# Optimization experiments

Hardware: AMD Instinct MI355X
Metric: run time of the kernel (lower is better)

## Reference

```python
import jax, jax.numpy as jnp
import numpy as np

N, F, H, E = 10000, 256, 256, 320000
TEMPERATURE = 1.0


def setup_inputs() -> dict:
    key = jax.random.key(0)
    k_x, k_ei, k_w1, k_b1, k_w2, k_b2 = jax.random.split(key, 6)
    x = jax.random.normal(k_x, (N, F), dtype=jnp.float32)
    edge_index = jax.random.randint(k_ei, (2, E), 0, N, dtype=jnp.int64)
    # PyTorch nn.Linear default init: U(-1/sqrt(fan_in), 1/sqrt(fan_in)), weight shape (out, in)
    lim1 = 1.0 / np.sqrt(2 * F)
    W1 = jax.random.uniform(k_w1, (H, 2 * F), dtype=jnp.float32, minval=-lim1, maxval=lim1)
    b1 = jax.random.uniform(k_b1, (H,), dtype=jnp.float32, minval=-lim1, maxval=lim1)
    lim2 = 1.0 / np.sqrt(H)
    W2 = jax.random.uniform(k_w2, (1, H), dtype=jnp.float32, minval=-lim2, maxval=lim2)
    b2 = jax.random.uniform(k_b2, (1,), dtype=jnp.float32, minval=-lim2, maxval=lim2)
    return {"x": x, "edge_index": edge_index, "W1": W1, "b1": b1, "W2": W2, "b2": b2}


def reference(x, edge_index, W1, b1, W2, b2):
    row, col = edge_index[0], edge_index[1]
    edge_feat = jnp.concatenate([x[row], x[col]], axis=-1)  # (E, 2F)
    h = jax.nn.relu(edge_feat @ W1.T + b1)                  # (E, H)
    logits = (h @ W2.T + b2).squeeze(-1)                    # (E,)
    m = jax.nn.sigmoid(logits / max(TEMPERATURE, 1e-6))
    return m
```

## Files before the change

kernel.cpp:

```cpp
#include <hip/hip_runtime.h>
#include <hip/hip_bf16.h>


typedef __attribute__((ext_vector_type(8))) short bf16x8;
typedef __attribute__((ext_vector_type(4))) float f32x4;

__device__ __forceinline__ unsigned short f2bf(float f) {
    __hip_bfloat16 h = __float2bfloat16(f);
    return *reinterpret_cast<unsigned short*>(&h);
}

__global__ __launch_bounds__(256) void convert_w(const float* __restrict__ w1,
                                                 unsigned short* __restrict__ wb,
                                                 int nw4) {
    int i = blockIdx.x * 256 + threadIdx.x;
    if (i < nw4) {
        float4 v = ((const float4*)w1)[i];
        ushort4 o = {f2bf(v.x), f2bf(v.y), f2bf(v.z), f2bf(v.w)};
        ((ushort4*)wb)[i] = o;
    }
}

__global__ __launch_bounds__(256) void gemm_mfma(const float* __restrict__ x,
                                                 const unsigned short* __restrict__ wb,
                                                 const float* __restrict__ b1,
                                                 unsigned short* __restrict__ uv,
                                                 int M) {
    __shared__ unsigned short As[2][16][40];

    const int t    = threadIdx.x;
    const int wave = t >> 6;
    const int lane = t & 63;
    const int lm   = lane & 15;
    const int lq   = lane >> 4;
    const int lk   = lq * 8;
    const int m0   = blockIdx.x * 16;

    const int srow = t >> 4;
    const int sk   = (t & 15) * 2;
    const int grow = m0 + srow;
    const float* sptr = x + (size_t)(grow < M ? grow : (M - 1)) * 256 + sk;

    const int half    = wave >> 1;
    const int colbase = wave * 128;
    const int rowbase = (wave & 1) * 128;
    const unsigned short* bpre =
        wb + (size_t)(rowbase + lm) * 512 + half * 256 + lk;

    f32x4 acc[8];
#pragma unroll
    for (int j = 0; j < 8; ++j) acc[j] = f32x4{0.f, 0.f, 0.f, 0.f};

    float2 apref = *(const float2*)(sptr);

#pragma unroll
    for (int it = 0; it < 8; ++it) {
        const int kt  = it * 32;
        const int cur = it & 1;

        unsigned int lo = ((unsigned int)f2bf(apref.x));
        unsigned int hi = ((unsigned int)f2bf(apref.y)) << 16;
        *(unsigned int*)&As[cur][srow][sk] = lo | hi;

        if (it < 7) apref = *(const float2*)(sptr + kt + 32);

        __syncthreads();

        bf16x8 a = *(const bf16x8*)&As[cur][lm][lk];

#pragma unroll
        for (int j = 0; j < 8; ++j) {
            bf16x8 b = *(const bf16x8*)(bpre + (size_t)j * 16 * 512 + kt);
            acc[j] = __builtin_amdgcn_mfma_f32_16x16x32_bf16(a, b, acc[j], 0, 0, 0);
        }
    }

    const int row0 = m0 + lq * 4;
#pragma unroll
    for (int j = 0; j < 8; ++j) {
        const int col  = colbase + j * 16 + lm;
        const float badd = half ? 0.f : b1[col];
#pragma unroll
        for (int r = 0; r < 4; ++r) {
            if (row0 + r < M)
                uv[(size_t)(row0 + r) * 512 + col] = f2bf(acc[j][r] + badd);
        }
    }
}

__global__ __launch_bounds__(256) void edge_kernel(const unsigned short* __restrict__ uv,
                                                   const int* __restrict__ ei,
                                                   const float* __restrict__ w2,
                                                   const float* __restrict__ b2p,
                                                   float* __restrict__ out, int E) {
    const int lane = threadIdx.x & 63;
    const int g = lane >> 4;
    const int c = lane & 15;
    const int wid = (blockIdx.x * blockDim.x + threadIdx.x) >> 6;
    const int nwav = (gridDim.x * blockDim.x) >> 6;
    const int nb = E >> 2;

    float w2r[16];
#pragma unroll
    for (int i = 0; i < 4; ++i)
        *(float4*)&w2r[i * 4] = *(const float4*)(w2 + c * 16 + i * 4);
    const float b2 = b2p[0];

    for (int b = wid; b < nb; b += nwav) {
        const int e = b * 4 + g;
        const int row = ei[e];
        const int col = ei[E + e];
        const unsigned int* up = (const unsigned int*)(uv + (size_t)row * 512 + c * 16);
        const unsigned int* vp = (const unsigned int*)(uv + (size_t)col * 512 + 256 + c * 16);

        unsigned int uw[8], vw[8];
        *(uint4*)&uw[0] = *(const uint4*)up;
        *(uint4*)&uw[4] = *(const uint4*)(up + 4);
        *(uint4*)&vw[0] = *(const uint4*)vp;
        *(uint4*)&vw[4] = *(const uint4*)(vp + 4);

        float2 p2 = {0.f, 0.f};
#pragma unroll
        for (int i = 0; i < 8; ++i) {
            float2 u2 = {__uint_as_float(uw[i] << 16),
                         __uint_as_float(uw[i] & 0xffff0000u)};
            float2 v2 = {__uint_as_float(vw[i] << 16),
                         __uint_as_float(vw[i] & 0xffff0000u)};
            float2 s2 = {u2.x + v2.x, u2.y + v2.y};
            s2.x = fmaxf(s2.x, 0.f);
            s2.y = fmaxf(s2.y, 0.f);
            p2.x = fmaf(s2.x, w2r[2 * i], p2.x);
            p2.y = fmaf(s2.y, w2r[2 * i + 1], p2.y);
        }
        float p = p2.x + p2.y;

#pragma unroll
        for (int off = 1; off < 16; off <<= 1)
            p += __shfl_xor(p, off, 64);

        if (c == 0) {
            out[e] = 1.f / (1.f + __expf(-(p + b2)));
        }
    }
}

extern "C" void kernel_launch(void* const* d_in, const int* in_sizes, int n_in,
                              void* d_out, int out_size, void* d_ws, size_t ws_size,
                              hipStream_t stream) {
    const float* x  = (const float*)d_in[0];
    const int*   ei = (const int*)d_in[1];
    const float* W1 = (const float*)d_in[2];
    const float* b1 = (const float*)d_in[3];
    const float* W2 = (const float*)d_in[4];
    const float* b2 = (const float*)d_in[5];
    float* out = (float*)d_out;

    const int N = in_sizes[0] / 256;
    const int E = in_sizes[1] / 2;

    unsigned short* uv = (unsigned short*)d_ws;
    unsigned short* wb = uv + (size_t)N * 512;

    const int nw4 = (256 * 512) / 4;
    convert_w<<<(nw4 + 255) / 256, 256, 0, stream>>>(W1, wb, nw4);

    gemm_mfma<<<(N + 15) / 16, 256, 0, stream>>>(x, wb, b1, uv, N);

    edge_kernel<<<2048, 256, 0, stream>>>(uv, ei, W2, b2, out, E);
}
```

Measured before the change: 131.0 us.

## Fuse weight convert, node GEMM and edge scoring into one cooperative kernel

Merges the three launches (weight bf16 conversion, per-node projection GEMM, per-edge scoring) into a single persistent cooperative kernel separated by grid-wide syncs. The GEMM becomes a grid-stride loop over row tiles. The edge loop now handles two edge batches per iteration so more gathers are in flight. This removes two launch gaps but adds grid.sync cost, and the persistent grid, which assumes 256 CUs, may be less occupied than the original per-kernel grids.

```diff
diff --git a/kernel.cpp b/kernel.cpp
--- a/kernel.cpp
+++ b/kernel.cpp
@@ -1,5 +1,8 @@
 #include <hip/hip_runtime.h>
 #include <hip/hip_bf16.h>
+#include <hip/hip_cooperative_groups.h>
+
+namespace cg = cooperative_groups;
 
 
 typedef __attribute__((ext_vector_type(8))) short bf16x8;
@@ -10,95 +13,87 @@
     return *reinterpret_cast<unsigned short*>(&h);
 }
 
-__global__ __launch_bounds__(256) void convert_w(const float* __restrict__ w1,
-                                                 unsigned short* __restrict__ wb,
-                                                 int nw4) {
-    int i = blockIdx.x * 256 + threadIdx.x;
-    if (i < nw4) {
-        float4 v = ((const float4*)w1)[i];
+__global__ __launch_bounds__(256, 4) void fused_kernel(
+        const float* __restrict__ x, const int* __restrict__ ei,
+        const float* __restrict__ W1, const float* __restrict__ b1,
+        const float* __restrict__ w2, const float* __restrict__ b2p,
+        float* __restrict__ out, unsigned short* __restrict__ uv,
+        unsigned short* __restrict__ wb, int M, int E) {
+    __shared__ __align__(16) unsigned short As[2][16][40];
+
+    cg::grid_group grid = cg::this_grid();
+    const int t   = threadIdx.x;
+    const int gid = blockIdx.x * 256 + t;
+
+    if (gid < 32768) {
+        float4 v = ((const float4*)W1)[gid];
         ushort4 o = {f2bf(v.x), f2bf(v.y), f2bf(v.z), f2bf(v.w)};
-        ((ushort4*)wb)[i] = o;
+        ((ushort4*)wb)[gid] = o;
     }
-}
-
-__global__ __launch_bounds__(256) void gemm_mfma(const float* __restrict__ x,
-                                                 const unsigned short* __restrict__ wb,
-                                                 const float* __restrict__ b1,
-                                                 unsigned short* __restrict__ uv,
-                                                 int M) {
-    __shared__ unsigned short As[2][16][40];
-
-    const int t    = threadIdx.x;
+    grid.sync();
+
     const int wave = t >> 6;
     const int lane = t & 63;
     const int lm   = lane & 15;
     const int lq   = lane >> 4;
     const int lk   = lq * 8;
-    const int m0   = blockIdx.x * 16;
-
     const int srow = t >> 4;
     const int sk   = (t & 15) * 2;
-    const int grow = m0 + srow;
-    const float* sptr = x + (size_t)(grow < M ? grow : (M - 1)) * 256 + sk;
-
     const int half    = wave >> 1;
     const int colbase = wave * 128;
     const int rowbase = (wave & 1) * 128;
     const unsigned short* bpre =
         wb + (size_t)(rowbase + lm) * 512 + half * 256 + lk;
 
-    f32x4 acc[8];
-#pragma unroll
-    for (int j = 0; j < 8; ++j) acc[j] = f32x4{0.f, 0.f, 0.f, 0.f};
-
-    float2 apref = *(const float2*)(sptr);
-
-#pragma unroll
-    for (int it = 0; it < 8; ++it) {
-        const int kt  = it * 32;
-        const int cur = it & 1;
-
-        unsigned int lo = ((unsigned int)f2bf(apref.x));
-        unsigned int hi = ((unsigned int)f2bf(apref.y)) << 16;
-        *(unsigned int*)&As[cur][srow][sk] = lo | hi;
-
-        if (it < 7) apref = *(const float2*)(sptr + kt + 32);
-
+    const int ntiles = (M + 15) / 16;
+    for (int mt = blockIdx.x; mt < ntiles; mt += gridDim.x) {
+        const int m0   = mt * 16;
+        const int grow = m0 + srow;
+        const float* sptr = x + (size_t)(grow < M ? grow : (M - 1)) * 256 + sk;
+
+        f32x4 acc[8];
+#pragma unroll
+        for (int j = 0; j < 8; ++j) acc[j] = f32x4{0.f, 0.f, 0.f, 0.f};
+
+        float2 apref = *(const float2*)(sptr);
+
+#pragma unroll
+        for (int it = 0; it < 8; ++it) {
+            const int kt  = it * 32;
+            const int cur = it & 1;
+            unsigned int lo = ((unsigned int)f2bf(apref.x));
+            unsigned int hi = ((unsigned int)f2bf(apref.y)) << 16;
+            *(unsigned int*)&As[cur][srow][sk] = lo | hi;
+            if (it < 7) apref = *(const float2*)(sptr + kt + 32);
+            __syncthreads();
+            bf16x8 a = *(const bf16x8*)&As[cur][lm][lk];
+#pragma unroll
+            for (int j = 0; j < 8; ++j) {
+                bf16x8 b = *(const bf16x8*)(bpre + (size_t)j * 16 * 512 + kt);
+                acc[j] = __builtin_amdgcn_mfma_f32_16x16x32_bf16(a, b, acc[j], 0, 0, 0);
+            }
+        }
+
+        const int row0 = m0 + lq * 4;
+#pragma unroll
+        for (int j = 0; j < 8; ++j) {
+            const int col  = colbase + j * 16 + lm;
+            const float badd = half ? 0.f : b1[col];
+#pragma unroll
+            for (int r = 0; r < 4; ++r) {
+                if (row0 + r < M)
+                    uv[(size_t)(row0 + r) * 512 + col] = f2bf(acc[j][r] + badd);
+            }
+        }
         __syncthreads();
-
-        bf16x8 a = *(const bf16x8*)&As[cur][lm][lk];
-
-#pragma unroll
-        for (int j = 0; j < 8; ++j) {
-            bf16x8 b = *(const bf16x8*)(bpre + (size_t)j * 16 * 512 + kt);
-            acc[j] = __builtin_amdgcn_mfma_f32_16x16x32_bf16(a, b, acc[j], 0, 0, 0);
-        }
     }
-
-    const int row0 = m0 + lq * 4;
-#pragma unroll
-    for (int j = 0; j < 8; ++j) {
-        const int col  = colbase + j * 16 + lm;
-        const float badd = half ? 0.f : b1[col];
-#pragma unroll
-        for (int r = 0; r < 4; ++r) {
-            if (row0 + r < M)
-                uv[(size_t)(row0 + r) * 512 + col] = f2bf(acc[j][r] + badd);
-        }
-    }
-}
-
-__global__ __launch_bounds__(256) void edge_kernel(const unsigned short* __restrict__ uv,
-                                                   const int* __restrict__ ei,
-                                                   const float* __restrict__ w2,
-                                                   const float* __restrict__ b2p,
-                                                   float* __restrict__ out, int E) {
-    const int lane = threadIdx.x & 63;
-    const int g = lane >> 4;
-    const int c = lane & 15;
-    const int wid = (blockIdx.x * blockDim.x + threadIdx.x) >> 6;
-    const int nwav = (gridDim.x * blockDim.x) >> 6;
-    const int nb = E >> 2;
+    grid.sync();
+
+    const int g = lq;
+    const int c = lm;
+    const int wid  = blockIdx.x * 4 + wave;
+    const int nwav = gridDim.x * 4;
+    const int nb   = E >> 2;
 
     float w2r[16];
 #pragma unroll
@@ -106,40 +101,69 @@
         *(float4*)&w2r[i * 4] = *(const float4*)(w2 + c * 16 + i * 4);
     const float b2 = b2p[0];
 
-    for (int b = wid; b < nb; b += nwav) {
-        const int e = b * 4 + g;
-        const int row = ei[e];
-        const int col = ei[E + e];
-        const unsigned int* up = (const unsigned int*)(uv + (size_t)row * 512 + c * 16);
-        const unsigned int* vp = (const unsigned int*)(uv + (size_t)col * 512 + 256 + c * 16);
+    for (int b = wid; b < nb; b += 2 * nwav) {
+        const int bB = b + nwav;
+        const bool has2 = bB < nb;
+
+        const int e0 = b * 4 + g;
+        const int r0 = ei[e0];
+        const int c0 = ei[E + e0];
+        const int e1 = has2 ? bB * 4 + g : e0;
+        const int r1 = ei[e1];
+        const int c1 = ei[E + e1];
+
+        const uint4* up0 = (const uint4*)(uv + (size_t)r0 * 512 + c * 16);
+        const uint4* vp0 = (const uint4*)(uv + (size_t)c0 * 512 + 256 + c * 16);
+        const uint4* up1 = (const uint4*)(uv + (size_t)r1 * 512 + c * 16);
+        const uint4* vp1 = (const uint4*)(uv + (size_t)c1 * 512 + 256 + c * 16);
+
+        uint4 ua0 = up0[0], ua1 = up0[1];
+        uint4 va0 = vp0[0], va1 = vp0[1];
+        uint4 ub0 = up1[0], ub1 = up1[1];
+        uint4 vb0 = vp1[0], vb1 = vp1[1];
 
         unsigned int uw[8], vw[8];
-        *(uint4*)&uw[0] = *(const uint4*)up;
-        *(uint4*)&uw[4] = *(const uint4*)(up + 4);
-        *(uint4*)&vw[0] = *(const uint4*)vp;
-        *(uint4*)&vw[4] = *(const uint4*)(vp + 4);
-
-        float2 p2 = {0.f, 0.f};
+        float2 p2;
+        float p;
+
+        *(uint4*)&uw[0] = ua0; *(uint4*)&uw[4] = ua1;
+        *(uint4*)&vw[0] = va0; *(uint4*)&vw[4] = va1;
+        p2 = float2{0.f, 0.f};
 #pragma unroll
         for (int i = 0; i < 8; ++i) {
             float2 u2 = {__uint_as_float(uw[i] << 16),
                          __uint_as_float(uw[i] & 0xffff0000u)};
             float2 v2 = {__uint_as_float(vw[i] << 16),
                          __uint_as_float(vw[i] & 0xffff0000u)};
-            float2 s2 = {u2.x + v2.x, u2.y + v2.y};
-            s2.x = fmaxf(s2.x, 0.f);
-            s2.y = fmaxf(s2.y, 0.f);
+            float2 s2 = {fmaxf(u2.x + v2.x, 0.f), fmaxf(u2.y + v2.y, 0.f)};
             p2.x = fmaf(s2.x, w2r[2 * i], p2.x);
             p2.y = fmaf(s2.y, w2r[2 * i + 1], p2.y);
         }
-        float p = p2.x + p2.y;
-
+        p = p2.x + p2.y;
 #pragma unroll
         for (int off = 1; off < 16; off <<= 1)
             p += __shfl_xor(p, off, 64);
-
-        if (c == 0) {
-            out[e] = 1.f / (1.f + __expf(-(p + b2)));
+        if (c == 0) out[e0] = 1.f / (1.f + __expf(-(p + b2)));
+
+        if (has2) {
+            *(uint4*)&uw[0] = ub0; *(uint4*)&uw[4] = ub1;
+            *(uint4*)&vw[0] = vb0; *(uint4*)&vw[4] = vb1;
+            p2 = float2{0.f, 0.f};
+#pragma unroll
+            for (int i = 0; i < 8; ++i) {
+                float2 u2 = {__uint_as_float(uw[i] << 16),
+                             __uint_as_float(uw[i] & 0xffff0000u)};
+                float2 v2 = {__uint_as_float(vw[i] << 16),
+                             __uint_as_float(vw[i] & 0xffff0000u)};
+                float2 s2 = {fmaxf(u2.x + v2.x, 0.f), fmaxf(u2.y + v2.y, 0.f)};
+                p2.x = fmaf(s2.x, w2r[2 * i], p2.x);
+                p2.y = fmaf(s2.y, w2r[2 * i + 1], p2.y);
+            }
+            p = p2.x + p2.y;
+#pragma unroll
+            for (int off = 1; off < 16; off <<= 1)
+                p += __shfl_xor(p, off, 64);
+            if (c == 0) out[e1] = 1.f / (1.f + __expf(-(p + b2)));
         }
     }
 }
@@ -155,16 +179,22 @@
     const float* b2 = (const float*)d_in[5];
     float* out = (float*)d_out;
 
-    const int N = in_sizes[0] / 256;
-    const int E = in_sizes[1] / 2;
+    int N = in_sizes[0] / 256;
+    int E = in_sizes[1] / 2;
 
     unsigned short* uv = (unsigned short*)d_ws;
     unsigned short* wb = uv + (size_t)N * 512;
 
-    const int nw4 = (256 * 512) / 4;
-    convert_w<<<(nw4 + 255) / 256, 256, 0, stream>>>(W1, wb, nw4);
-
-    gemm_mfma<<<(N + 15) / 16, 256, 0, stream>>>(x, wb, b1, uv, N);
-
-    edge_kernel<<<2048, 256, 0, stream>>>(uv, ei, W2, b2, out, E);
+    int maxBlk = 0;
+    hipOccupancyMaxActiveBlocksPerMultiprocessor(&maxBlk, (const void*)fused_kernel,
+                                                 256, 0);
+    if (maxBlk < 1) maxBlk = 1;
+    if (maxBlk > 8) maxBlk = 8;
+    int grid = maxBlk * 256;
+
+    void* args[] = {(void*)&x, (void*)&ei, (void*)&W1, (void*)&b1, (void*)&W2,
+                    (void*)&b2, (void*)&out, (void*)&uv, (void*)&wb,
+                    (void*)&N, (void*)&E};
+    hipLaunchCooperativeKernel((void*)fused_kernel, dim3(grid), dim3(256),
+                               args, 0, stream);
 }
```

Result: slower. 288.1 us (+119.9%).

## Bucket-sort edges by source row before edge scoring for gather locality

Applied to the files above, without the earlier changes.

Adds a cooperative counting-sort kernel that groups edges into 16-row buckets by source node and writes sorted row, col and original-index arrays. The edge kernel then handles contiguous blocks of sorted edges per wave, so rows of the uv table are reused in cache, and scatters results back through the original index. This costs an extra kernel with two grid syncs, extra index reads, and a scattered output write.

```diff
diff --git a/kernel.cpp b/kernel.cpp
--- a/kernel.cpp
+++ b/kernel.cpp
@@ -1,5 +1,8 @@
 #include <hip/hip_runtime.h>
 #include <hip/hip_bf16.h>
+#include <hip/hip_cooperative_groups.h>
+
+namespace cg = cooperative_groups;
 
 
 typedef __attribute__((ext_vector_type(8))) short bf16x8;
@@ -8,6 +11,72 @@
 __device__ __forceinline__ unsigned short f2bf(float f) {
     __hip_bfloat16 h = __float2bfloat16(f);
     return *reinterpret_cast<unsigned short*>(&h);
+}
+
+#define NBUCK 625
+#define NBPAD 640
+#define SORTB 80
+#define CHUNK 4000
+
+__global__ __launch_bounds__(640) void sort_kernel(const int* __restrict__ ei,
+                                                   int* __restrict__ hist,
+                                                   int* __restrict__ srow,
+                                                   int* __restrict__ scol,
+                                                   int* __restrict__ sidx, int E) {
+    __shared__ int lh[NBPAD];
+    cg::grid_group grid = cg::this_grid();
+    const int t = threadIdx.x;
+    const int b = blockIdx.x;
+    const int e0 = b * CHUNK;
+    const int e1 = (e0 + CHUNK < E) ? e0 + CHUNK : E;
+
+    if (t < NBPAD) lh[t] = 0;
+    __syncthreads();
+    for (int e = e0 + t; e < e1; e += 640)
+        atomicAdd(&lh[ei[e] >> 4], 1);
+    __syncthreads();
+    if (t < NBPAD) hist[t * SORTB + b] = lh[t];
+
+    grid.sync();
+
+    if (b == 0) {
+        __shared__ int tot[NBPAD];
+        if (t < NBPAD) {
+            int s = 0;
+#pragma unroll 4
+            for (int bb = 0; bb < SORTB; ++bb) {
+                int v = hist[t * SORTB + bb];
+                hist[t * SORTB + bb] = s;
+                s += v;
+            }
+            tot[t] = s;
+        }
+        __syncthreads();
+        for (int d = 1; d < NBPAD; d <<= 1) {
+            int v = (t < NBPAD && t >= d) ? tot[t - d] : 0;
+            __syncthreads();
+            if (t < NBPAD) tot[t] += v;
+            __syncthreads();
+        }
+        if (t < NBPAD) {
+            int base = (t == 0) ? 0 : tot[t - 1];
+#pragma unroll 4
+            for (int bb = 0; bb < SORTB; ++bb)
+                hist[t * SORTB + bb] += base;
+        }
+    }
+
+    grid.sync();
+
+    if (t < NBPAD) lh[t] = hist[t * SORTB + b];
+    __syncthreads();
+    for (int e = e0 + t; e < e1; e += 640) {
+        int row = ei[e];
+        int pos = atomicAdd(&lh[row >> 4], 1);
+        srow[pos] = row;
+        scol[pos] = ei[E + e];
+        sidx[pos] = e;
+    }
 }
 
 __global__ __launch_bounds__(256) void convert_w(const float* __restrict__ w1,
@@ -26,7 +95,7 @@
                                                  const float* __restrict__ b1,
                                                  unsigned short* __restrict__ uv,
                                                  int M) {
-    __shared__ unsigned short As[2][16][40];
+    __shared__ __align__(16) unsigned short As[2][16][40];
 
     const int t    = threadIdx.x;
     const int wave = t >> 6;
@@ -57,17 +126,12 @@
     for (int it = 0; it < 8; ++it) {
         const int kt  = it * 32;
         const int cur = it & 1;
-
         unsigned int lo = ((unsigned int)f2bf(apref.x));
         unsigned int hi = ((unsigned int)f2bf(apref.y)) << 16;
         *(unsigned int*)&As[cur][srow][sk] = lo | hi;
-
         if (it < 7) apref = *(const float2*)(sptr + kt + 32);
-
         __syncthreads();
-
         bf16x8 a = *(const bf16x8*)&As[cur][lm][lk];
-
 #pragma unroll
         for (int j = 0; j < 8; ++j) {
             bf16x8 b = *(const bf16x8*)(bpre + (size_t)j * 16 * 512 + kt);
@@ -89,16 +153,19 @@
 }
 
 __global__ __launch_bounds__(256) void edge_kernel(const unsigned short* __restrict__ uv,
-                                                   const int* __restrict__ ei,
+                                                   const int* __restrict__ srowp,
+                                                   const int* __restrict__ scolp,
+                                                   const int* __restrict__ sidxp,
                                                    const float* __restrict__ w2,
                                                    const float* __restrict__ b2p,
                                                    float* __restrict__ out, int E) {
     const int lane = threadIdx.x & 63;
     const int g = lane >> 4;
     const int c = lane & 15;
-    const int wid = (blockIdx.x * blockDim.x + threadIdx.x) >> 6;
-    const int nwav = (gridDim.x * blockDim.x) >> 6;
-    const int nb = E >> 2;
+    const int wave = threadIdx.x >> 6;
+    const int nb   = E >> 2;
+    const int bpw  = 10;
+    const int base = (blockIdx.x * 4 + wave) * bpw;
 
     float w2r[16];
 #pragma unroll
@@ -106,31 +173,33 @@
         *(float4*)&w2r[i * 4] = *(const float4*)(w2 + c * 16 + i * 4);
     const float b2 = b2p[0];
 
-    for (int b = wid; b < nb; b += nwav) {
-        const int e = b * 4 + g;
-        const int row = ei[e];
-        const int col = ei[E + e];
-        const unsigned int* up = (const unsigned int*)(uv + (size_t)row * 512 + c * 16);
-        const unsigned int* vp = (const unsigned int*)(uv + (size_t)col * 512 + 256 + c * 16);
+    for (int i = 0; i < bpw; ++i) {
+        const int b = base + i;
+        if (b >= nb) break;
+        const int p0 = b * 4 + g;
+        const int row = srowp[p0];
+        const int col = scolp[p0];
+        const int idx = sidxp[p0];
+
+        const uint4* up = (const uint4*)(uv + (size_t)row * 512 + c * 16);
+        const uint4* vp = (const uint4*)(uv + (size_t)col * 512 + 256 + c * 16);
+        uint4 u0 = up[0], u1 = up[1];
+        uint4 v0 = vp[0], v1 = vp[1];
 
         unsigned int uw[8], vw[8];
-        *(uint4*)&uw[0] = *(const uint4*)up;
-        *(uint4*)&uw[4] = *(const uint4*)(up + 4);
-        *(uint4*)&vw[0] = *(const uint4*)vp;
-        *(uint4*)&vw[4] = *(const uint4*)(vp + 4);
+        *(uint4*)&uw[0] = u0; *(uint4*)&uw[4] = u1;
+        *(uint4*)&vw[0] = v0; *(uint4*)&vw[4] = v1;
 
         float2 p2 = {0.f, 0.f};
 #pragma unroll
-        for (int i = 0; i < 8; ++i) {
-            float2 u2 = {__uint_as_float(uw[i] << 16),
-                         __uint_as_float(uw[i] & 0xffff0000u)};
-            float2 v2 = {__uint_as_float(vw[i] << 16),
-                         __uint_as_float(vw[i] & 0xffff0000u)};
-            float2 s2 = {u2.x + v2.x, u2.y + v2.y};
-            s2.x = fmaxf(s2.x, 0.f);
-            s2.y = fmaxf(s2.y, 0.f);
-            p2.x = fmaf(s2.x, w2r[2 * i], p2.x);
-            p2.y = fmaf(s2.y, w2r[2 * i + 1], p2.y);
+        for (int j = 0; j < 8; ++j) {
+            float2 u2 = {__uint_as_float(uw[j] << 16),
+                         __uint_as_float(uw[j] & 0xffff0000u)};
+            float2 v2 = {__uint_as_float(vw[j] << 16),
+                         __uint_as_float(vw[j] & 0xffff0000u)};
+            float2 s2 = {fmaxf(u2.x + v2.x, 0.f), fmaxf(u2.y + v2.y, 0.f)};
+            p2.x = fmaf(s2.x, w2r[2 * j], p2.x);
+            p2.y = fmaf(s2.y, w2r[2 * j + 1], p2.y);
         }
         float p = p2.x + p2.y;
 
@@ -138,9 +207,7 @@
         for (int off = 1; off < 16; off <<= 1)
             p += __shfl_xor(p, off, 64);
 
-        if (c == 0) {
-            out[e] = 1.f / (1.f + __expf(-(p + b2)));
-        }
+        if (c == 0) out[idx] = 1.f / (1.f + __expf(-(p + b2)));
     }
 }
 
@@ -155,16 +222,25 @@
     const float* b2 = (const float*)d_in[5];
     float* out = (float*)d_out;
 
-    const int N = in_sizes[0] / 256;
-    const int E = in_sizes[1] / 2;
+    int N = in_sizes[0] / 256;
+    int E = in_sizes[1] / 2;
 
     unsigned short* uv = (unsigned short*)d_ws;
     unsigned short* wb = uv + (size_t)N * 512;
+    int* hist = (int*)(wb + 256 * 512);
+    int* srow = hist + NBPAD * SORTB;
+    int* scol = srow + E;
+    int* sidx = scol + E;
+
+    void* sargs[] = {(void*)&ei, (void*)&hist, (void*)&srow, (void*)&scol,
+                     (void*)&sidx, (void*)&E};
+    hipLaunchCooperativeKernel((void*)sort_kernel, dim3(SORTB), dim3(640),
+                               sargs, 0, stream);
 
     const int nw4 = (256 * 512) / 4;
     convert_w<<<(nw4 + 255) / 256, 256, 0, stream>>>(W1, wb, nw4);
 
     gemm_mfma<<<(N + 15) / 16, 256, 0, stream>>>(x, wb, b1, uv, N);
 
-    edge_kernel<<<2048, 256, 0, stream>>>(uv, ei, W2, b2, out, E);
-}
+    edge_kernel<<<2048, 256, 0, stream>>>(uv, srow, scol, sidx, W2, b2, out, E);
+}
```

New measurement: 225.3 us. 1.72x slower.
